# Optimization experiments

Measured on AMD Instinct MI355X. Metric: run time of the kernel, lower is better.

The kernel has to match this reference:

```python
import jax, jax.numpy as jnp
import numpy as np
import math

B, T, D, N = 4, 1024, 768, 7  # batch, seq, d_model, n_chambers
STEP, WARMUP = 4000, 2000      # curriculum: step past warmup -> all masks ~1
INIT_SCALE = 0.01


def _curriculum_masks():
    # NautilusScheduler.get_masks: smooth sigmoid activation per chamber (static floats)
    slope = 8.0 * N / WARMUP
    return [1.0 / (1.0 + math.exp(-slope * (STEP - WARMUP * (i + 0.5) / N))) for i in range(N)]


def _layernorm(x, g, b, eps=1e-5):
    m = jnp.mean(x, axis=-1, keepdims=True)
    v = jnp.mean((x - m) ** 2, axis=-1, keepdims=True)
    return (x - m) * jax.lax.rsqrt(v + eps) * g + b


def _chamber(h, Wq, Wk, gw, gb, sp, mask_val, causal):
    # get_bias stand-in: bilinear content bias (B,T,T)
    q = h @ Wq                                   # (B,T,D)
    k = h @ Wk                                   # (B,T,D)
    bias = jnp.einsum('btd,bsd->bts', q, k) / jnp.sqrt(jnp.asarray(D, h.dtype))
    bias = jnp.where(causal[None], bias, -jnp.inf)   # causal masked_fill
    w = jnp.nan_to_num(jax.nn.softmax(bias, axis=-1))
    enrichment = jnp.einsum('bts,bsd->btd', w, h) - h
    gate = jax.nn.sigmoid(h @ gw[:, None] + gb)      # (B,T,1)
    scale = jax.nn.softplus(sp)                      # learnable positive scale
    return scale * gate * mask_val * enrichment


def setup_inputs() -> dict:
    key = jax.random.key(0)
    ks = jax.random.split(key, 8)
    x = jax.random.normal(ks[0], (B, T, D), jnp.float32)
    s = 1.0 / np.sqrt(D)
    Wq = jax.random.normal(ks[1], (N, D, D), jnp.float32) * s
    Wk = jax.random.normal(ks[2], (N, D, D), jnp.float32) * s
    gate_w = jax.random.normal(ks[3], (N, D), jnp.float32) * 0.02
    gate_b = jnp.zeros((N,), jnp.float32)
    # per-chamber softplus-inverse init: log(exp(init*(1+3*prog))-1+1e-6)
    sp = np.array([math.log(math.exp(INIT_SCALE * (1.0 + 3.0 * i / (N - 1))) - 1.0 + 1e-6)
                   for i in range(N)], dtype=np.float32)
    scale_p = jnp.asarray(sp)
    merge_W = jax.random.normal(ks[4], (D, N * D), jnp.float32) * (1.0 / np.sqrt(N * D))
    return {
        'x': x, 'Wq': Wq, 'Wk': Wk, 'gate_w': gate_w, 'gate_b': gate_b,
        'scale_p': scale_p, 'merge_W': merge_W,
        'mode_logit': jnp.float32(0.0), 'residual_gate': jnp.float32(0.1),
        'ln_pre_g': jnp.ones((D,), jnp.float32), 'ln_pre_b': jnp.zeros((D,), jnp.float32),
        'ln_post_g': jnp.ones((D,), jnp.float32), 'ln_post_b': jnp.zeros((D,), jnp.float32),
    }


def reference(x, Wq, Wk, gate_w, gate_b, scale_p, merge_W, mode_logit,
              residual_gate, ln_pre_g, ln_pre_b, ln_post_g, ln_post_b):
    masks = _curriculum_masks()
    causal = jnp.tril(jnp.ones((T, T), bool))
    h = _layernorm(x, ln_pre_g, ln_pre_b)
    mode_gate = jax.nn.sigmoid(mode_logit)
    seq = jnp.zeros_like(h)
    deltas = []
    for i in range(N):  # fixed small structural loop over chambers
        seq = seq + _chamber(h + seq, Wq[i], Wk[i], gate_w[i], gate_b[i],
                             scale_p[i], masks[i], causal)
        deltas.append(_chamber(h, Wq[i], Wk[i], gate_w[i], gate_b[i],
                               scale_p[i], masks[i], causal))
    par = jnp.concatenate(deltas, axis=-1) @ merge_W.T  # (B,T,D)
    enrichment = (1.0 - mode_gate) * seq + mode_gate * par
    enrichment = _layernorm(enrichment, ln_post_g, ln_post_b)
    return x + residual_gate * enrichment
```

## Files before the change

### kernel.cpp

```cpp
#include <hip/hip_runtime.h>
#include <hip/hip_bf16.h>
#include <math.h>

#define D_MODEL 768
#define T_SEQ   1024
#define BATCH   4
#define NCH     7
#define ROWS    4096
#define KM      (NCH * D_MODEL)

typedef unsigned short u16;
typedef __attribute__((ext_vector_type(8))) short bh8;
typedef __attribute__((ext_vector_type(4))) float f32x4;

__device__ __forceinline__ u16 f2bf(float f) {
    union { float f; unsigned u; } v; v.f = f;
    return (u16)((v.u + 0x7fffu + ((v.u >> 16) & 1u)) >> 16);
}
__device__ __forceinline__ float bf2f(u16 b) {
    union { unsigned u; float f; } v; v.u = ((unsigned)b) << 16;
    return v.f;
}
__device__ __forceinline__ float wred_sum(float v) {
    #pragma unroll
    for (int o = 32; o; o >>= 1) v += __shfl_down(v, o, 64);
    return v;
}
__device__ __forceinline__ float wred_max(float v) {
    #pragma unroll
    for (int o = 32; o; o >>= 1) v = fmaxf(v, __shfl_down(v, o, 64));
    return v;
}
__device__ __forceinline__ float chamber_mask(int i) {
    float slope = 8.0f * 7.0f / 2000.0f;
    return 1.0f / (1.0f + __expf(-slope * (4000.0f - 2000.0f * (i + 0.5f) / 7.0f)));
}

#define GLD16(g, l) __builtin_amdgcn_global_load_lds( \
    (const __attribute__((address_space(1))) void*)(g), \
    (__attribute__((address_space(3))) void*)(l), 16, 0, 0)

__device__ __forceinline__ int xcd_swizzle(int gflat, int Ntot) {
    if ((Ntot & 7) == 0) {
        int chunk = Ntot >> 3;
        gflat = (gflat & 7) * chunk + (gflat >> 3);
    }
    return gflat;
}

__global__ __launch_bounds__(256)
void gemm_nt_kernel(const u16* __restrict__ A, const u16* __restrict__ B,
                    void* __restrict__ Cv,
                    int K, int lda, int ldb, int ldc,
                    long long sA1, long long sA2, long long sB1, long long sB2,
                    long long sC1, long long sC2, int zm,
                    float alpha, int mode, int causal_skip, int causal_k,
                    int kss, int klen)
{
    int gx = gridDim.x, gy = gridDim.y;
    int Ntot = gx * gy * gridDim.z;
    int gflat = xcd_swizzle(blockIdx.x + gx * (blockIdx.y + gy * blockIdx.z), Ntot);
    int bn = gflat % gx;
    int rest = gflat / gx;
    int bm = rest % gy;
    int bz = rest / gy;
    if (causal_skip && bn > bm) return;
    int bz1 = bz % zm, bz2 = bz / zm;

    const u16* Ab = A + bz1 * sA1 + bz2 * sA2 + (long long)(bm * 128) * lda;
    const u16* Bb = B + bz1 * sB1 + bz2 * sB2 + (long long)(bn * 128) * ldb;

    __shared__ u16 sm[4 * 128 * 32];
    u16* Al0 = sm;
    u16* Bl0 = sm + 128 * 32;
    u16* Al1 = sm + 2 * 128 * 32;
    u16* Bl1 = sm + 3 * 128 * 32;

    int tid  = threadIdx.x;
    int lane = tid & 63;
    int wave = tid >> 6;
    int wm = wave >> 1, wn = wave & 1;

    int k_begin = kss ? bz1 * kss : 0;
    int k_end   = klen ? (k_begin + klen) : K;
    if (causal_k) k_end = min(k_end, (bm + 1) * 128);

    f32x4 acc[4][4];
    #pragma unroll
    for (int i = 0; i < 4; i++)
        #pragma unroll
        for (int j = 0; j < 4; j++)
            acc[i][j] = (f32x4){0.f, 0.f, 0.f, 0.f};

    int srow = lane >> 2;
    int skq  = (lane & 3) * 8;
    int fm   = lane & 15;
    int fk   = (lane >> 4) * 8;

    for (int k0 = k_begin; k0 < k_end; k0 += 64) {
        __syncthreads();
        #pragma unroll
        for (int r = 0; r < 2; r++) {
            int row = r * 64 + wave * 16 + srow;
            long long ra = (long long)row * lda + k0 + skq;
            long long rb2 = (long long)row * ldb + k0 + skq;
            GLD16(Ab + ra,       Al0 + row * 32 + skq);
            GLD16(Bb + rb2,      Bl0 + row * 32 + skq);
            GLD16(Ab + ra + 32,  Al1 + row * 32 + skq);
            GLD16(Bb + rb2 + 32, Bl1 + row * 32 + skq);
        }
        __syncthreads();

        #pragma unroll
        for (int p = 0; p < 2; p++) {
            const u16* Al = p ? Al1 : Al0;
            const u16* Bl = p ? Bl1 : Bl0;
            bh8 af[4], bf[4];
            #pragma unroll
            for (int i = 0; i < 4; i++)
                af[i] = *(const bh8*)(Al + (wm * 64 + i * 16 + fm) * 32 + fk);
            #pragma unroll
            for (int j = 0; j < 4; j++)
                bf[j] = *(const bh8*)(Bl + (wn * 64 + j * 16 + fm) * 32 + fk);
            #pragma unroll
            for (int i = 0; i < 4; i++)
                #pragma unroll
                for (int j = 0; j < 4; j++)
                    acc[i][j] = __builtin_amdgcn_mfma_f32_16x16x32_bf16(af[i], bf[j], acc[i][j], 0, 0, 0);
        }
    }

    int rbase = bm * 128 + wm * 64 + (lane >> 4) * 4;
    int cbase = bn * 128 + wn * 64 + (lane & 15);
    long long zoff = bz1 * sC1 + bz2 * sC2;
    if (mode == 1) {
        u16* C = (u16*)Cv + zoff;
        #pragma unroll
        for (int i = 0; i < 4; i++)
            #pragma unroll
            for (int j = 0; j < 4; j++)
                #pragma unroll
                for (int r = 0; r < 4; r++)
                    C[(long long)(rbase + i * 16 + r) * ldc + cbase + j * 16] = f2bf(acc[i][j][r] * alpha);
    } else if (mode == 3) {
        u16* C = (u16*)Cv + zoff;
        #pragma unroll
        for (int i = 0; i < 4; i++)
            #pragma unroll
            for (int j = 0; j < 4; j++)
                #pragma unroll
                for (int r = 0; r < 4; r++) {
                    union { _Float16 h; u16 u; } cv;
                    cv.h = (_Float16)(acc[i][j][r] * alpha);
                    C[(long long)(rbase + i * 16 + r) * ldc + cbase + j * 16] = cv.u;
                }
    } else {
        float* C = (float*)Cv + zoff;
        #pragma unroll
        for (int i = 0; i < 4; i++)
            #pragma unroll
            for (int j = 0; j < 4; j++)
                #pragma unroll
                for (int r = 0; r < 4; r++)
                    C[(long long)(rbase + i * 16 + r) * ldc + cbase + j * 16] = acc[i][j][r] * alpha;
    }
}

__global__ __launch_bounds__(256)
void gemm64_nt_kernel(const u16* __restrict__ A, const u16* __restrict__ B,
                      void* __restrict__ Cv,
                      int K, int lda, int ldb, int ldc,
                      long long sA1, long long sA2, long long sB1, long long sB2,
                      long long sC1, long long sC2, int zm,
                      float alpha, int mode, int causal_skip, int causal_k,
                      float* __restrict__ hhfp, const float* __restrict__ coefp,
                      u16* __restrict__ hbsp, u16* __restrict__ htsp,
                      const float* __restrict__ hp, u16* __restrict__ dbp)
{
    int gx = gridDim.x, gy = gridDim.y;
    int Ntot = gx * gy * gridDim.z;
    int gflat = xcd_swizzle(blockIdx.x + gx * (blockIdx.y + gy * blockIdx.z), Ntot);
    int bn = gflat % gx;
    int rest = gflat / gx;
    int bm = rest % gy;
    int bz = rest / gy;
    if (causal_skip && bn > bm) return;
    int bz1 = bz % zm, bz2 = bz / zm;

    const u16* Ab = A + bz1 * sA1 + bz2 * sA2 + (long long)(bm * 64) * lda;
    const u16* Bb = B + bz1 * sB1 + bz2 * sB2 + (long long)(bn * 64) * ldb;

    __shared__ u16 sm[8 * 64 * 32];
    const int PS = 64 * 32;

    int tid  = threadIdx.x;
    int lane = tid & 63;
    int wave = tid >> 6;

    int k_end = causal_k ? min(K, (bm + 1) * 64) : K;

    f32x4 acc[4];
    #pragma unroll
    for (int j = 0; j < 4; j++) acc[j] = (f32x4){0.f, 0.f, 0.f, 0.f};

    int srow   = tid >> 2;
    int schunk = (tid & 3) * 8;
    int fm     = lane & 15;
    int fk     = (lane >> 4) * 8;

    int k0 = 0;
    while (k0 < k_end) {
        __syncthreads();
        if (k_end - k0 >= 128) {
            #pragma unroll
            for (int p = 0; p < 4; p++) {
                long long ra  = (long long)srow * lda + k0 + p * 32 + schunk;
                long long rb2 = (long long)srow * ldb + k0 + p * 32 + schunk;
                GLD16(Ab + ra,  sm + (2 * p) * PS + srow * 32 + schunk);
                GLD16(Bb + rb2, sm + (2 * p + 1) * PS + srow * 32 + schunk);
            }
            __syncthreads();
            #pragma unroll
            for (int p = 0; p < 4; p++) {
                const u16* Al = sm + (2 * p) * PS;
                const u16* Bl = sm + (2 * p + 1) * PS;
                bh8 af = *(const bh8*)(Al + (wave * 16 + fm) * 32 + fk);
                bh8 bf[4];
                #pragma unroll
                for (int j = 0; j < 4; j++)
                    bf[j] = *(const bh8*)(Bl + (j * 16 + fm) * 32 + fk);
                #pragma unroll
                for (int j = 0; j < 4; j++)
                    acc[j] = __builtin_amdgcn_mfma_f32_16x16x32_bf16(af, bf[j], acc[j], 0, 0, 0);
            }
            k0 += 128;
        } else {
            #pragma unroll
            for (int p = 0; p < 2; p++) {
                long long ra  = (long long)srow * lda + k0 + p * 32 + schunk;
                long long rb2 = (long long)srow * ldb + k0 + p * 32 + schunk;
                GLD16(Ab + ra,  sm + (2 * p) * PS + srow * 32 + schunk);
                GLD16(Bb + rb2, sm + (2 * p + 1) * PS + srow * 32 + schunk);
            }
            __syncthreads();
            #pragma unroll
            for (int p = 0; p < 2; p++) {
                const u16* Al = sm + (2 * p) * PS;
                const u16* Bl = sm + (2 * p + 1) * PS;
                bh8 af = *(const bh8*)(Al + (wave * 16 + fm) * 32 + fk);
                bh8 bf[4];
                #pragma unroll
                for (int j = 0; j < 4; j++)
                    bf[j] = *(const bh8*)(Bl + (j * 16 + fm) * 32 + fk);
                #pragma unroll
                for (int j = 0; j < 4; j++)
                    acc[j] = __builtin_amdgcn_mfma_f32_16x16x32_bf16(af, bf[j], acc[j], 0, 0, 0);
            }
            k0 += 64;
        }
    }

    int rbase = bm * 64 + wave * 16 + (lane >> 4) * 4;
    int cbase = bn * 64 + (lane & 15);
    long long zoff = bz1 * sC1 + bz2 * sC2;
    if (mode == 1) {
        u16* C = (u16*)Cv + zoff;
        #pragma unroll
        for (int j = 0; j < 4; j++)
            #pragma unroll
            for (int r = 0; r < 4; r++)
                C[(long long)(rbase + r) * ldc + cbase + j * 16] = f2bf(acc[j][r] * alpha);
    } else if (mode == 3) {
        u16* C = (u16*)Cv + zoff;
        #pragma unroll
        for (int j = 0; j < 4; j++)
            #pragma unroll
            for (int r = 0; r < 4; r++) {
                union { _Float16 h; u16 u; } cv;
                cv.h = (_Float16)(acc[j][r] * alpha);
                C[(long long)(rbase + r) * ldc + cbase + j * 16] = cv.u;
            }
    } else if (mode == 5) {
        int b = bz1, ch = bz2;
        #pragma unroll
        for (int r = 0; r < 4; r++) {
            int t = rbase + r;
            long long rowg = (long long)b * T_SEQ + t;
            float cf = coefp[(long long)ch * ROWS + rowg];
            #pragma unroll
            for (int j = 0; j < 4; j++) {
                int d = cbase + j * 16;
                float hv = hp[rowg * D_MODEL + d];
                dbp[rowg * KM + ch * D_MODEL + d] = f2bf(cf * (acc[j][r] - hv));
            }
        }
    } else if (mode == 6) {
        __syncthreads();
        u16* tile = sm;
        #pragma unroll
        for (int r = 0; r < 4; r++) {
            int t = rbase + r;
            long long rowg = (long long)bz1 * T_SEQ + t;
            float cf = coefp[rowg];
            int tl = t - bm * 64;
            #pragma unroll
            for (int j = 0; j < 4; j++) {
                int d = cbase + j * 16;
                long long idx = rowg * D_MODEL + d;
                float v = hhfp[idx];
                float nh = v + cf * (acc[j][r] - v);
                hhfp[idx] = nh;
                u16 w = f2bf(nh);
                hbsp[idx] = w;
                tile[((lane & 15) + j * 16) * 66 + tl] = w;
            }
        }
        __syncthreads();
        int dl = tid >> 2, tch = (tid & 3) * 16;
        long long ob = (long long)bz1 * T_SEQ * D_MODEL +
                       (long long)(bn * 64 + dl) * T_SEQ + bm * 64 + tch;
        #pragma unroll
        for (int kk = 0; kk < 16; kk++)
            htsp[ob + kk] = tile[dl * 66 + tch + kk];
    } else {
        float* C = (float*)Cv + zoff;
        #pragma unroll
        for (int j = 0; j < 4; j++)
            #pragma unroll
            for (int r = 0; r < 4; r++)
                C[(long long)(rbase + r) * ldc + cbase + j * 16] = acc[j][r] * alpha;
    }
}

__global__ __launch_bounds__(256)
void ln_pre_kernel(const float* __restrict__ x, const float* __restrict__ g,
                   const float* __restrict__ b, float* __restrict__ h,
                   float* __restrict__ hhf, u16* __restrict__ hbp,
                   u16* __restrict__ hbs)
{
    int row = blockIdx.x;
    long long base = (long long)row * D_MODEL;
    int tid = threadIdx.x, lane = tid & 63, wave = tid >> 6;
    __shared__ float red[4];
    float v[3]; float s = 0.f;
    #pragma unroll
    for (int k = 0; k < 3; k++) { v[k] = x[base + tid + k * 256]; s += v[k]; }
    s = wred_sum(s);
    if (lane == 0) red[wave] = s;
    __syncthreads();
    float mean = (red[0] + red[1] + red[2] + red[3]) * (1.f / D_MODEL);
    __syncthreads();
    float sq = 0.f;
    #pragma unroll
    for (int k = 0; k < 3; k++) { float dd = v[k] - mean; sq += dd * dd; }
    sq = wred_sum(sq);
    if (lane == 0) red[wave] = sq;
    __syncthreads();
    float var = (red[0] + red[1] + red[2] + red[3]) * (1.f / D_MODEL);
    float rstd = rsqrtf(var + 1e-5f);
    #pragma unroll
    for (int k = 0; k < 3; k++) {
        int c = tid + k * 256;
        float o = (v[k] - mean) * rstd * g[c] + b[c];
        h[base + c] = o; hhf[base + c] = o;
        u16 w = f2bf(o);
        hbp[base + c] = w; hbs[base + c] = w;
    }
}

__global__ __launch_bounds__(256)
void transpose2_kernel(const u16* __restrict__ hb, u16* __restrict__ htp,
                       u16* __restrict__ hts)
{
    __shared__ u16 tile[32][33];
    int b = blockIdx.z;
    int d0 = blockIdx.x * 32, t0 = blockIdx.y * 32;
    int tx = threadIdx.x & 31, ty = threadIdx.x >> 5;
    long long bb = (long long)b * T_SEQ * D_MODEL;
    #pragma unroll
    for (int i = 0; i < 32; i += 8)
        tile[ty + i][tx] = hb[bb + (long long)(t0 + ty + i) * D_MODEL + d0 + tx];
    __syncthreads();
    #pragma unroll
    for (int i = 0; i < 32; i += 8) {
        long long o = bb + (long long)(d0 + ty + i) * T_SEQ + t0 + tx;
        u16 w = tile[tx][ty + i];
        htp[o] = w; hts[o] = w;
    }
}

__device__ __forceinline__ void softmax_row(u16* row, int len, int tid, int lane, int wave,
                                            float* red)
{
    float ev[4];
    float m = -3.0e38f;
    #pragma unroll
    for (int k = 0; k < 4; k++) {
        int s = tid + k * 256;
        if (s < len) {
            union { u16 u; _Float16 h; } cv; cv.u = row[s];
            ev[k] = (float)cv.h;
        } else ev[k] = -3.0e38f;
        m = fmaxf(m, ev[k]);
    }
    m = wred_max(m);
    if (lane == 0) red[wave] = m;
    __syncthreads();
    m = fmaxf(fmaxf(red[0], red[1]), fmaxf(red[2], red[3]));
    __syncthreads();
    float sum = 0.f;
    #pragma unroll
    for (int k = 0; k < 4; k++) {
        int s = tid + k * 256;
        float e = (s < len) ? __expf(ev[k] - m) : 0.f;
        ev[k] = e; sum += e;
    }
    sum = wred_sum(sum);
    if (lane == 0) red[wave] = sum;
    __syncthreads();
    sum = red[0] + red[1] + red[2] + red[3];
    float inv = 1.f / sum;
    #pragma unroll
    for (int k = 0; k < 4; k++)
        row[tid + k * 256] = f2bf(ev[k] * inv);
}

__global__ __launch_bounds__(256)
void softmax_kernel(u16* __restrict__ SP)
{
    int t = blockIdx.x, z = blockIdx.y;
    __shared__ float red[4];
    int tid = threadIdx.x, lane = tid & 63, wave = tid >> 6;
    softmax_row(SP + (long long)z * T_SEQ * T_SEQ + (long long)t * T_SEQ,
                t + 1, tid, lane, wave, red);
}

__global__ __launch_bounds__(256)
void softmax_coef_kernel(u16* __restrict__ SP, const float* __restrict__ hhf,
                         const float* __restrict__ gw, const float* __restrict__ gb,
                         const float* __restrict__ sp, int ci,
                         float* __restrict__ coefS)
{
    int t = blockIdx.x, z = blockIdx.y;
    int tid = threadIdx.x, lane = tid & 63, wave = tid >> 6;
    if (z == BATCH) {
        int row = t * 4 + wave;
        long long base = (long long)row * D_MODEL;
        const float* g = gw + ci * D_MODEL;
        float dot = 0.f;
        #pragma unroll
        for (int k = 0; k < 12; k++) dot += hhf[base + lane + 64 * k] * g[lane + 64 * k];
        dot = wred_sum(dot);
        if (lane == 0) {
            float gate = 1.f / (1.f + __expf(-(dot + gb[ci])));
            coefS[row] = log1pf(expf(sp[ci])) * chamber_mask(ci) * gate;
        }
        return;
    }
    __shared__ float red[4];
    softmax_row(SP + (long long)z * T_SEQ * T_SEQ + (long long)t * T_SEQ,
                t + 1, tid, lane, wave, red);
}

__global__ __launch_bounds__(256)
void coef_par_kernel(const float* __restrict__ h, const float* __restrict__ gw,
                     const float* __restrict__ gb, const float* __restrict__ sp,
                     float* __restrict__ coefP)
{
    int row = blockIdx.x * 4 + (threadIdx.x >> 6);
    int lane = threadIdx.x & 63;
    long long base = (long long)row * D_MODEL;
    float hv[12];
    #pragma unroll
    for (int k = 0; k < 12; k++) hv[k] = h[base + lane + 64 * k];
    for (int ci = 0; ci < NCH; ci++) {
        const float* g = gw + ci * D_MODEL;
        float dot = 0.f;
        #pragma unroll
        for (int k = 0; k < 12; k++) dot += hv[k] * g[lane + 64 * k];
        dot = wred_sum(dot);
        if (lane == 0) {
            float gate = 1.f / (1.f + __expf(-(dot + gb[ci])));
            coefP[ci * ROWS + row] = log1pf(expf(sp[ci])) * chamber_mask(ci) * gate;
        }
    }
}

__global__ __launch_bounds__(256)
void cast4_kernel(const float4* __restrict__ in, ushort4* __restrict__ outp, int n4)
{
    int i = blockIdx.x * 256 + threadIdx.x;
    if (i < n4) {
        float4 v = in[i];
        ushort4 o;
        o.x = f2bf(v.x); o.y = f2bf(v.y); o.z = f2bf(v.z); o.w = f2bf(v.w);
        outp[i] = o;
    }
}

__global__ __launch_bounds__(256)
void final_kernel(const float* __restrict__ x, const float* __restrict__ h,
                  const float* __restrict__ hhf, const u16* __restrict__ Pp,
                  const float* __restrict__ mode_logit, const float* __restrict__ residual_gate,
                  const float* __restrict__ g, const float* __restrict__ b,
                  float* __restrict__ out)
{
    const long long RDe = (long long)ROWS * D_MODEL;
    int row = blockIdx.x;
    long long base = (long long)row * D_MODEL;
    int tid = threadIdx.x, lane = tid & 63, wave = tid >> 6;
    __shared__ float red[4];
    float mg = 1.f / (1.f + __expf(-mode_logit[0]));
    float rg = residual_gate[0];
    float e[3]; float s = 0.f;
    #pragma unroll
    for (int k = 0; k < 3; k++) {
        int c = tid + k * 256;
        float p = 0.f;
        #pragma unroll
        for (int z = 0; z < NCH; z++) p += bf2f(Pp[z * RDe + base + c]);
        float v = (1.f - mg) * (hhf[base + c] - h[base + c]) + mg * p;
        e[k] = v; s += v;
    }
    s = wred_sum(s);
    if (lane == 0) red[wave] = s;
    __syncthreads();
    float mean = (red[0] + red[1] + red[2] + red[3]) * (1.f / D_MODEL);
    __syncthreads();
    float sq = 0.f;
    #pragma unroll
    for (int k = 0; k < 3; k++) { float dd = e[k] - mean; sq += dd * dd; }
    sq = wred_sum(sq);
    if (lane == 0) red[wave] = sq;
    __syncthreads();
    float var = (red[0] + red[1] + red[2] + red[3]) * (1.f / D_MODEL);
    float rstd = rsqrtf(var + 1e-5f);
    #pragma unroll
    for (int k = 0; k < 3; k++) {
        int c = tid + k * 256;
        out[base + c] = x[base + c] + rg * ((e[k] - mean) * rstd * g[c] + b[c]);
    }
}

extern "C" void kernel_launch(void* const* d_in, const int* in_sizes, int n_in,
                              void* d_out, int out_size, void* d_ws, size_t ws_size,
                              hipStream_t stream)
{
    (void)in_sizes; (void)n_in; (void)out_size; (void)ws_size;
    const float* x             = (const float*)d_in[0];
    const float* Wq            = (const float*)d_in[1];
    const float* Wk            = (const float*)d_in[2];
    const float* gate_w        = (const float*)d_in[3];
    const float* gate_b        = (const float*)d_in[4];
    const float* scale_p       = (const float*)d_in[5];
    const float* merge_W       = (const float*)d_in[6];
    const float* mode_logit    = (const float*)d_in[7];
    const float* residual_gate = (const float*)d_in[8];
    const float* ln_pre_g      = (const float*)d_in[9];
    const float* ln_pre_b      = (const float*)d_in[10];
    const float* ln_post_g     = (const float*)d_in[11];
    const float* ln_post_b     = (const float*)d_in[12];
    float* out = (float*)d_out;

    const long long DD  = (long long)D_MODEL * D_MODEL;
    const long long TD  = (long long)T_SEQ * D_MODEL;
    const long long TTs = (long long)T_SEQ * T_SEQ;
    const long long RDe = (long long)ROWS * D_MODEL;

    size_t off = 0;
    char* wsb = (char*)d_ws;
    auto alloc = [&](size_t bytes) -> void* {
        void* p = wsb + off; off += (bytes + 255) & ~(size_t)255; return p;
    };
    u16*   Mtb  = (u16*)alloc((size_t)NCH * DD * 2);
    u16*   mgb  = (u16*)alloc((size_t)D_MODEL * KM * 2);
    float* h    = (float*)alloc(RDe * 4);
    float* hhf  = (float*)alloc(RDe * 4);
    u16*   hbp  = (u16*)alloc(RDe * 2);
    u16*   htp  = (u16*)alloc(RDe * 2);
    u16*   hbs  = (u16*)alloc(RDe * 2);
    u16*   hts0 = (u16*)alloc(RDe * 2);
    u16*   hts1 = (u16*)alloc(RDe * 2);
    u16*   Spar = (u16*)alloc((size_t)(NCH * BATCH) * TTs * 2);
    u16*   Sseq = (u16*)alloc((size_t)BATCH * TTs * 2);
    u16*   Upar = (u16*)alloc((size_t)NCH * RDe * 2);
    u16*   Useq = (u16*)alloc(RDe * 2);
    u16*   db   = (u16*)alloc((size_t)ROWS * KM * 2);
    float* coefP= (float*)alloc((size_t)NCH * ROWS * 4);
    float* coefS= (float*)alloc((size_t)ROWS * 4);
    u16*   Wqb  = Spar;
    u16*   Wkb  = Spar + (size_t)NCH * DD;
    u16*   Pp   = Upar;

    const float sc = 1.0f / sqrtf((float)D_MODEL);
    const int N4W = (int)((size_t)NCH * DD) / 4;
    const int N4M = (int)((size_t)D_MODEL * KM) / 4;

    ln_pre_kernel<<<ROWS, 256, 0, stream>>>(x, ln_pre_g, ln_pre_b, h, hhf, hbp, hbs);
    cast4_kernel<<<(N4W + 255) / 256, 256, 0, stream>>>((const float4*)Wq, (ushort4*)Wqb, N4W);
    cast4_kernel<<<(N4W + 255) / 256, 256, 0, stream>>>((const float4*)Wk, (ushort4*)Wkb, N4W);
    cast4_kernel<<<(N4M + 255) / 256, 256, 0, stream>>>((const float4*)merge_W, (ushort4*)mgb, N4M);
    transpose2_kernel<<<dim3(24, 32, BATCH), 256, 0, stream>>>(hbp, htp, hts0);
    coef_par_kernel<<<ROWS / 4, 256, 0, stream>>>(h, gate_w, gate_b, scale_p, coefP);

    gemm_nt_kernel<<<dim3(6, 6, NCH), 256, 0, stream>>>(
        Wkb, Wqb, Mtb, D_MODEL, D_MODEL, D_MODEL, D_MODEL,
        DD, 0, DD, 0, DD, 0, NCH, 1.f, 1, 0, 0, 0, 0);

    gemm_nt_kernel<<<dim3(6, 32, NCH), 256, 0, stream>>>(
        hbp, Mtb, Upar, D_MODEL, D_MODEL, D_MODEL, D_MODEL,
        0, 0, DD, 0, RDe, 0, NCH, 1.f, 1, 0, 0, 0, 0);
    gemm64_nt_kernel<<<dim3(16, 16, BATCH * NCH), 256, 0, stream>>>(
        Upar, hbp, Spar, D_MODEL, D_MODEL, D_MODEL, T_SEQ,
        TD, RDe, TD, 0, TTs, 4 * TTs, BATCH, sc, 3, 1, 0,
        nullptr, nullptr, nullptr, nullptr, nullptr, nullptr);
    softmax_kernel<<<dim3(T_SEQ, BATCH * NCH), 256, 0, stream>>>(Spar);
    gemm64_nt_kernel<<<dim3(12, 16, BATCH * NCH), 256, 0, stream>>>(
        Spar, htp, nullptr, T_SEQ, T_SEQ, T_SEQ, D_MODEL,
        TTs, 4 * TTs, TD, 0, 0, 0, BATCH, 1.f, 5, 0, 1,
        nullptr, coefP, nullptr, nullptr, h, db);
    gemm_nt_kernel<<<dim3(6, 32, NCH), 256, 0, stream>>>(
        db, mgb, Pp, KM, KM, KM, D_MODEL,
        0, 0, 0, 0, RDe, 0, NCH, 1.f, 1, 0, 0, D_MODEL, D_MODEL);

    u16* htsCur = hts0;
    u16* htsNxt = hts1;
    for (int i = 0; i < NCH; i++) {
        gemm64_nt_kernel<<<dim3(12, 64, 1), 256, 0, stream>>>(
            hbs, Mtb + (long long)i * DD, Useq,
            D_MODEL, D_MODEL, D_MODEL, D_MODEL, 0, 0, 0, 0, 0, 0, 1,
            1.f, 1, 0, 0, nullptr, nullptr, nullptr, nullptr, nullptr, nullptr);
        gemm64_nt_kernel<<<dim3(16, 16, BATCH), 256, 0, stream>>>(
            Useq, hbs, Sseq, D_MODEL, D_MODEL, D_MODEL, T_SEQ,
            TD, 0, TD, 0, TTs, 0, BATCH, sc, 3, 1, 0,
            nullptr, nullptr, nullptr, nullptr, nullptr, nullptr);
        softmax_coef_kernel<<<dim3(T_SEQ, BATCH + 1), 256, 0, stream>>>(
            Sseq, hhf, gate_w, gate_b, scale_p, i, coefS);
        gemm64_nt_kernel<<<dim3(12, 16, BATCH), 256, 0, stream>>>(
            Sseq, htsCur, nullptr, T_SEQ, T_SEQ, T_SEQ, D_MODEL,
            TTs, 0, TD, 0, 0, 0, BATCH, 1.f, 6, 0, 1,
            hhf, coefS, hbs, htsNxt, nullptr, nullptr);
        u16* tmp = htsCur; htsCur = htsNxt; htsNxt = tmp;
    }

    final_kernel<<<ROWS, 256, 0, stream>>>(x, h, hhf, Pp, mode_logit, residual_gate,
                                           ln_post_g, ln_post_b, out);
}
```

Baseline: 790.8 us.

## Interleave parallel-branch chamber GEMMs into sequential-loop launches via multi-descriptor kernels

Replaces the separate batched parallel-branch launches (U, scores, softmax, PV, merge) with per-chamber slices that are co-launched inside the sequential chamber loop. New gemm128_tri/gemm64_tri kernels take up to three GEMM descriptors and route block ids to each one, so the small, latency-bound sequential GEMMs share a grid with independent parallel work. The merge GEMM is split per chamber and lagged by one iteration. The goal is better GPU occupancy during the serial dependency chain and fewer launches. In exchange the merge GEMM runs as smaller pieces and the parallel work is spread across more launches.

```diff
diff --git a/kernel.cpp b/kernel.cpp
--- a/kernel.cpp
+++ b/kernel.cpp
@@ -1,5 +1,4 @@
 #include <hip/hip_runtime.h>
-#include <hip/hip_bf16.h>
 #include <math.h>
 
 #define D_MODEL 768
@@ -48,29 +47,44 @@
     return gflat;
 }
 
-__global__ __launch_bounds__(256)
-void gemm_nt_kernel(const u16* __restrict__ A, const u16* __restrict__ B,
-                    void* __restrict__ Cv,
-                    int K, int lda, int ldb, int ldc,
-                    long long sA1, long long sA2, long long sB1, long long sB2,
-                    long long sC1, long long sC2, int zm,
-                    float alpha, int mode, int causal_skip, int causal_k,
-                    int kss, int klen)
-{
-    int gx = gridDim.x, gy = gridDim.y;
-    int Ntot = gx * gy * gridDim.z;
-    int gflat = xcd_swizzle(blockIdx.x + gx * (blockIdx.y + gy * blockIdx.z), Ntot);
-    int bn = gflat % gx;
-    int rest = gflat / gx;
-    int bm = rest % gy;
-    int bz = rest / gy;
-    if (causal_skip && bn > bm) return;
-    int bz1 = bz % zm, bz2 = bz / zm;
-
-    const u16* Ab = A + bz1 * sA1 + bz2 * sA2 + (long long)(bm * 128) * lda;
-    const u16* Bb = B + bz1 * sB1 + bz2 * sB2 + (long long)(bn * 128) * ldb;
-
-    __shared__ u16 sm[4 * 128 * 32];
+struct GDesc {
+    const u16* A; const u16* B; void* C;
+    const float* coef;
+    const float* hfrz;
+    float* hhf;
+    u16* hbs;
+    u16* hts;
+    u16* db;
+    long long sA1, sB1, sC1;
+    int K, lda, ldb, ldc;
+    int gx, gy, gz;
+    int mode, cskip, ck;
+    float alpha;
+};
+
+__device__ __forceinline__ bool g_route(const GDesc& d, int& id,
+                                        int& bn, int& bm, int& bz)
+{
+    int n = d.gx * d.gy * d.gz;
+    if (id < n) {
+        int s = xcd_swizzle(id, n);
+        bn = s % d.gx;
+        int r = s / d.gx;
+        bm = r % d.gy;
+        bz = r / d.gy;
+        return true;
+    }
+    id -= n;
+    return false;
+}
+
+__device__ void g128_body(const GDesc& d, u16* sm, int bn, int bm, int bz)
+{
+    if (d.cskip && bn > bm) return;
+
+    const u16* Ab = d.A + bz * d.sA1 + (long long)(bm * 128) * d.lda;
+    const u16* Bb = d.B + bz * d.sB1 + (long long)(bn * 128) * d.ldb;
+
     u16* Al0 = sm;
     u16* Bl0 = sm + 128 * 32;
     u16* Al1 = sm + 2 * 128 * 32;
@@ -81,9 +95,7 @@
     int wave = tid >> 6;
     int wm = wave >> 1, wn = wave & 1;
 
-    int k_begin = kss ? bz1 * kss : 0;
-    int k_end   = klen ? (k_begin + klen) : K;
-    if (causal_k) k_end = min(k_end, (bm + 1) * 128);
+    int k_end = d.ck ? min(d.K, (bm + 1) * 128) : d.K;
 
     f32x4 acc[4][4];
     #pragma unroll
@@ -97,13 +109,13 @@
     int fm   = lane & 15;
     int fk   = (lane >> 4) * 8;
 
-    for (int k0 = k_begin; k0 < k_end; k0 += 64) {
+    for (int k0 = 0; k0 < k_end; k0 += 64) {
         __syncthreads();
         #pragma unroll
         for (int r = 0; r < 2; r++) {
             int row = r * 64 + wave * 16 + srow;
-            long long ra = (long long)row * lda + k0 + skq;
-            long long rb2 = (long long)row * ldb + k0 + skq;
+            long long ra  = (long long)row * d.lda + k0 + skq;
+            long long rb2 = (long long)row * d.ldb + k0 + skq;
             GLD16(Ab + ra,       Al0 + row * 32 + skq);
             GLD16(Bb + rb2,      Bl0 + row * 32 + skq);
             GLD16(Ab + ra + 32,  Al1 + row * 32 + skq);
@@ -132,72 +144,52 @@
 
     int rbase = bm * 128 + wm * 64 + (lane >> 4) * 4;
     int cbase = bn * 128 + wn * 64 + (lane & 15);
-    long long zoff = bz1 * sC1 + bz2 * sC2;
-    if (mode == 1) {
-        u16* C = (u16*)Cv + zoff;
+    long long zoff = (long long)bz * d.sC1;
+    if (d.mode == 1) {
+        u16* C = (u16*)d.C + zoff;
         #pragma unroll
         for (int i = 0; i < 4; i++)
             #pragma unroll
             for (int j = 0; j < 4; j++)
                 #pragma unroll
                 for (int r = 0; r < 4; r++)
-                    C[(long long)(rbase + i * 16 + r) * ldc + cbase + j * 16] = f2bf(acc[i][j][r] * alpha);
-    } else if (mode == 3) {
-        u16* C = (u16*)Cv + zoff;
-        #pragma unroll
-        for (int i = 0; i < 4; i++)
-            #pragma unroll
-            for (int j = 0; j < 4; j++)
-                #pragma unroll
-                for (int r = 0; r < 4; r++) {
-                    union { _Float16 h; u16 u; } cv;
-                    cv.h = (_Float16)(acc[i][j][r] * alpha);
-                    C[(long long)(rbase + i * 16 + r) * ldc + cbase + j * 16] = cv.u;
-                }
+                    C[(long long)(rbase + i * 16 + r) * d.ldc + cbase + j * 16] = f2bf(acc[i][j][r] * d.alpha);
     } else {
-        float* C = (float*)Cv + zoff;
+        float* C = (float*)d.C + zoff;
         #pragma unroll
         for (int i = 0; i < 4; i++)
             #pragma unroll
             for (int j = 0; j < 4; j++)
                 #pragma unroll
                 for (int r = 0; r < 4; r++)
-                    C[(long long)(rbase + i * 16 + r) * ldc + cbase + j * 16] = acc[i][j][r] * alpha;
-    }
-}
-
-__global__ __launch_bounds__(256)
-void gemm64_nt_kernel(const u16* __restrict__ A, const u16* __restrict__ B,
-                      void* __restrict__ Cv,
-                      int K, int lda, int ldb, int ldc,
-                      long long sA1, long long sA2, long long sB1, long long sB2,
-                      long long sC1, long long sC2, int zm,
-                      float alpha, int mode, int causal_skip, int causal_k,
-                      float* __restrict__ hhfp, const float* __restrict__ coefp,
-                      u16* __restrict__ hbsp, u16* __restrict__ htsp,
-                      const float* __restrict__ hp, u16* __restrict__ dbp)
-{
-    int gx = gridDim.x, gy = gridDim.y;
-    int Ntot = gx * gy * gridDim.z;
-    int gflat = xcd_swizzle(blockIdx.x + gx * (blockIdx.y + gy * blockIdx.z), Ntot);
-    int bn = gflat % gx;
-    int rest = gflat / gx;
-    int bm = rest % gy;
-    int bz = rest / gy;
-    if (causal_skip && bn > bm) return;
-    int bz1 = bz % zm, bz2 = bz / zm;
-
-    const u16* Ab = A + bz1 * sA1 + bz2 * sA2 + (long long)(bm * 64) * lda;
-    const u16* Bb = B + bz1 * sB1 + bz2 * sB2 + (long long)(bn * 64) * ldb;
-
-    __shared__ u16 sm[8 * 64 * 32];
+                    C[(long long)(rbase + i * 16 + r) * d.ldc + cbase + j * 16] = acc[i][j][r] * d.alpha;
+    }
+}
+
+__global__ __launch_bounds__(256)
+void gemm128_tri(GDesc d0, GDesc d1, GDesc d2)
+{
+    __shared__ u16 sm[4 * 128 * 32];
+    int id = blockIdx.x, bn, bm, bz;
+    if (g_route(d0, id, bn, bm, bz)) { g128_body(d0, sm, bn, bm, bz); return; }
+    if (g_route(d1, id, bn, bm, bz)) { g128_body(d1, sm, bn, bm, bz); return; }
+    if (g_route(d2, id, bn, bm, bz)) { g128_body(d2, sm, bn, bm, bz); return; }
+}
+
+__device__ void g64_body(const GDesc& d, u16* sm, int bn, int bm, int bz)
+{
+    if (d.cskip && bn > bm) return;
+
+    const u16* Ab = d.A + bz * d.sA1 + (long long)(bm * 64) * d.lda;
+    const u16* Bb = d.B + bz * d.sB1 + (long long)(bn * 64) * d.ldb;
+
     const int PS = 64 * 32;
 
     int tid  = threadIdx.x;
     int lane = tid & 63;
     int wave = tid >> 6;
 
-    int k_end = causal_k ? min(K, (bm + 1) * 64) : K;
+    int k_end = d.ck ? min(d.K, (bm + 1) * 64) : d.K;
 
     f32x4 acc[4];
     #pragma unroll
@@ -214,8 +206,8 @@
         if (k_end - k0 >= 128) {
             #pragma unroll
             for (int p = 0; p < 4; p++) {
-                long long ra  = (long long)srow * lda + k0 + p * 32 + schunk;
-                long long rb2 = (long long)srow * ldb + k0 + p * 32 + schunk;
+                long long ra  = (long long)srow * d.lda + k0 + p * 32 + schunk;
+                long long rb2 = (long long)srow * d.ldb + k0 + p * 32 + schunk;
                 GLD16(Ab + ra,  sm + (2 * p) * PS + srow * 32 + schunk);
                 GLD16(Bb + rb2, sm + (2 * p + 1) * PS + srow * 32 + schunk);
             }
@@ -237,8 +229,8 @@
         } else {
             #pragma unroll
             for (int p = 0; p < 2; p++) {
-                long long ra  = (long long)srow * lda + k0 + p * 32 + schunk;
-                long long rb2 = (long long)srow * ldb + k0 + p * 32 + schunk;
+                long long ra  = (long long)srow * d.lda + k0 + p * 32 + schunk;
+                long long rb2 = (long long)srow * d.ldb + k0 + p * 32 + schunk;
                 GLD16(Ab + ra,  sm + (2 * p) * PS + srow * 32 + schunk);
                 GLD16(Bb + rb2, sm + (2 * p + 1) * PS + srow * 32 + schunk);
             }
@@ -262,74 +254,83 @@
 
     int rbase = bm * 64 + wave * 16 + (lane >> 4) * 4;
     int cbase = bn * 64 + (lane & 15);
-    long long zoff = bz1 * sC1 + bz2 * sC2;
-    if (mode == 1) {
-        u16* C = (u16*)Cv + zoff;
+    long long zoff = (long long)bz * d.sC1;
+    if (d.mode == 1) {
+        u16* C = (u16*)d.C + zoff;
         #pragma unroll
         for (int j = 0; j < 4; j++)
             #pragma unroll
             for (int r = 0; r < 4; r++)
-                C[(long long)(rbase + r) * ldc + cbase + j * 16] = f2bf(acc[j][r] * alpha);
-    } else if (mode == 3) {
-        u16* C = (u16*)Cv + zoff;
+                C[(long long)(rbase + r) * d.ldc + cbase + j * 16] = f2bf(acc[j][r] * d.alpha);
+    } else if (d.mode == 3) {
+        u16* C = (u16*)d.C + zoff;
         #pragma unroll
         for (int j = 0; j < 4; j++)
             #pragma unroll
             for (int r = 0; r < 4; r++) {
                 union { _Float16 h; u16 u; } cv;
-                cv.h = (_Float16)(acc[j][r] * alpha);
-                C[(long long)(rbase + r) * ldc + cbase + j * 16] = cv.u;
+                cv.h = (_Float16)(acc[j][r] * d.alpha);
+                C[(long long)(rbase + r) * d.ldc + cbase + j * 16] = cv.u;
             }
-    } else if (mode == 5) {
-        int b = bz1, ch = bz2;
+    } else if (d.mode == 5) {
         #pragma unroll
         for (int r = 0; r < 4; r++) {
             int t = rbase + r;
-            long long rowg = (long long)b * T_SEQ + t;
-            float cf = coefp[(long long)ch * ROWS + rowg];
+            long long rowg = (long long)bz * T_SEQ + t;
+            float cf = d.coef[rowg];
             #pragma unroll
             for (int j = 0; j < 4; j++) {
-                int d = cbase + j * 16;
-                float hv = hp[rowg * D_MODEL + d];
-                dbp[rowg * KM + ch * D_MODEL + d] = f2bf(cf * (acc[j][r] - hv));
+                int dc = cbase + j * 16;
+                float hv = d.hfrz[rowg * D_MODEL + dc];
+                d.db[rowg * KM + dc] = f2bf(cf * (acc[j][r] - hv));
             }
         }
-    } else if (mode == 6) {
+    } else if (d.mode == 6) {
         __syncthreads();
         u16* tile = sm;
         #pragma unroll
         for (int r = 0; r < 4; r++) {
             int t = rbase + r;
-            long long rowg = (long long)bz1 * T_SEQ + t;
-            float cf = coefp[rowg];
+            long long rowg = (long long)bz * T_SEQ + t;
+            float cf = d.coef[rowg];
             int tl = t - bm * 64;
             #pragma unroll
             for (int j = 0; j < 4; j++) {
-                int d = cbase + j * 16;
-                long long idx = rowg * D_MODEL + d;
-                float v = hhfp[idx];
+                int dc = cbase + j * 16;
+                long long idx = rowg * D_MODEL + dc;
+                float v = d.hhf[idx];
                 float nh = v + cf * (acc[j][r] - v);
-                hhfp[idx] = nh;
+                d.hhf[idx] = nh;
                 u16 w = f2bf(nh);
-                hbsp[idx] = w;
+                d.hbs[idx] = w;
                 tile[((lane & 15) + j * 16) * 66 + tl] = w;
             }
         }
         __syncthreads();
         int dl = tid >> 2, tch = (tid & 3) * 16;
-        long long ob = (long long)bz1 * T_SEQ * D_MODEL +
+        long long ob = (long long)bz * T_SEQ * D_MODEL +
                        (long long)(bn * 64 + dl) * T_SEQ + bm * 64 + tch;
         #pragma unroll
         for (int kk = 0; kk < 16; kk++)
-            htsp[ob + kk] = tile[dl * 66 + tch + kk];
+            d.hts[ob + kk] = tile[dl * 66 + tch + kk];
     } else {
-        float* C = (float*)Cv + zoff;
+        float* C = (float*)d.C + zoff;
         #pragma unroll
         for (int j = 0; j < 4; j++)
             #pragma unroll
             for (int r = 0; r < 4; r++)
-                C[(long long)(rbase + r) * ldc + cbase + j * 16] = acc[j][r] * alpha;
-    }
+                C[(long long)(rbase + r) * d.ldc + cbase + j * 16] = acc[j][r] * d.alpha;
+    }
+}
+
+__global__ __launch_bounds__(256)
+void gemm64_tri(GDesc d0, GDesc d1, GDesc d2)
+{
+    __shared__ u16 sm[8 * 64 * 32];
+    int id = blockIdx.x, bn, bm, bz;
+    if (g_route(d0, id, bn, bm, bz)) { g64_body(d0, sm, bn, bm, bz); return; }
+    if (g_route(d1, id, bn, bm, bz)) { g64_body(d1, sm, bn, bm, bz); return; }
+    if (g_route(d2, id, bn, bm, bz)) { g64_body(d2, sm, bn, bm, bz); return; }
 }
 
 __global__ __launch_bounds__(256)
@@ -426,24 +427,16 @@
 }
 
 __global__ __launch_bounds__(256)
-void softmax_kernel(u16* __restrict__ SP)
-{
-    int t = blockIdx.x, z = blockIdx.y;
-    __shared__ float red[4];
-    int tid = threadIdx.x, lane = tid & 63, wave = tid >> 6;
-    softmax_row(SP + (long long)z * T_SEQ * T_SEQ + (long long)t * T_SEQ,
-                t + 1, tid, lane, wave, red);
-}
-
-__global__ __launch_bounds__(256)
-void softmax_coef_kernel(u16* __restrict__ SP, const float* __restrict__ hhf,
-                         const float* __restrict__ gw, const float* __restrict__ gb,
-                         const float* __restrict__ sp, int ci,
-                         float* __restrict__ coefS)
-{
+void softmax9_kernel(u16* __restrict__ Sseq, u16* __restrict__ SparI,
+                     const float* __restrict__ hhf, const float* __restrict__ gw,
+                     const float* __restrict__ gb, const float* __restrict__ sp,
+                     int ci, float* __restrict__ coefS)
+{
+    const long long TTs = (long long)T_SEQ * T_SEQ;
     int t = blockIdx.x, z = blockIdx.y;
     int tid = threadIdx.x, lane = tid & 63, wave = tid >> 6;
-    if (z == BATCH) {
+    __shared__ float red[4];
+    if (z == 4) {
         int row = t * 4 + wave;
         long long base = (long long)row * D_MODEL;
         const float* g = gw + ci * D_MODEL;
@@ -457,9 +450,9 @@
         }
         return;
     }
-    __shared__ float red[4];
-    softmax_row(SP + (long long)z * T_SEQ * T_SEQ + (long long)t * T_SEQ,
-                t + 1, tid, lane, wave, red);
+    u16* base = (z < 4) ? (Sseq + (long long)z * TTs)
+                        : (SparI + (long long)(z - 5) * TTs);
+    softmax_row(base + (long long)t * T_SEQ, t + 1, tid, lane, wave, red);
 }
 
 __global__ __launch_bounds__(256)
@@ -596,6 +589,20 @@
     const int N4W = (int)((size_t)NCH * DD) / 4;
     const int N4M = (int)((size_t)D_MODEL * KM) / 4;
 
+    auto mkg = [](const u16* A, const u16* B, void* C,
+                  long long sA1, long long sB1, long long sC1,
+                  int K, int lda, int ldb, int ldc,
+                  int gx, int gy, int gz, int mode, int cskip, int ck, float alpha) {
+        GDesc d{};
+        d.A = A; d.B = B; d.C = C;
+        d.sA1 = sA1; d.sB1 = sB1; d.sC1 = sC1;
+        d.K = K; d.lda = lda; d.ldb = ldb; d.ldc = ldc;
+        d.gx = gx; d.gy = gy; d.gz = gz;
+        d.mode = mode; d.cskip = cskip; d.ck = ck; d.alpha = alpha;
+        return d;
+    };
+    GDesc ez{};
+
     ln_pre_kernel<<<ROWS, 256, 0, stream>>>(x, ln_pre_g, ln_pre_b, h, hhf, hbp, hbs);
     cast4_kernel<<<(N4W + 255) / 256, 256, 0, stream>>>((const float4*)Wq, (ushort4*)Wqb, N4W);
     cast4_kernel<<<(N4W + 255) / 256, 256, 0, stream>>>((const float4*)Wk, (ushort4*)Wkb, N4W);
@@ -603,44 +610,53 @@
     transpose2_kernel<<<dim3(24, 32, BATCH), 256, 0, stream>>>(hbp, htp, hts0);
     coef_par_kernel<<<ROWS / 4, 256, 0, stream>>>(h, gate_w, gate_b, scale_p, coefP);
 
-    gemm_nt_kernel<<<dim3(6, 6, NCH), 256, 0, stream>>>(
-        Wkb, Wqb, Mtb, D_MODEL, D_MODEL, D_MODEL, D_MODEL,
-        DD, 0, DD, 0, DD, 0, NCH, 1.f, 1, 0, 0, 0, 0);
-
-    gemm_nt_kernel<<<dim3(6, 32, NCH), 256, 0, stream>>>(
-        hbp, Mtb, Upar, D_MODEL, D_MODEL, D_MODEL, D_MODEL,
-        0, 0, DD, 0, RDe, 0, NCH, 1.f, 1, 0, 0, 0, 0);
-    gemm64_nt_kernel<<<dim3(16, 16, BATCH * NCH), 256, 0, stream>>>(
-        Upar, hbp, Spar, D_MODEL, D_MODEL, D_MODEL, T_SEQ,
-        TD, RDe, TD, 0, TTs, 4 * TTs, BATCH, sc, 3, 1, 0,
-        nullptr, nullptr, nullptr, nullptr, nullptr, nullptr);
-    softmax_kernel<<<dim3(T_SEQ, BATCH * NCH), 256, 0, stream>>>(Spar);
-    gemm64_nt_kernel<<<dim3(12, 16, BATCH * NCH), 256, 0, stream>>>(
-        Spar, htp, nullptr, T_SEQ, T_SEQ, T_SEQ, D_MODEL,
-        TTs, 4 * TTs, TD, 0, 0, 0, BATCH, 1.f, 5, 0, 1,
-        nullptr, coefP, nullptr, nullptr, h, db);
-    gemm_nt_kernel<<<dim3(6, 32, NCH), 256, 0, stream>>>(
-        db, mgb, Pp, KM, KM, KM, D_MODEL,
-        0, 0, 0, 0, RDe, 0, NCH, 1.f, 1, 0, 0, D_MODEL, D_MODEL);
+    {
+        GDesc dmt = mkg(Wkb, Wqb, Mtb, DD, DD, DD,
+                        D_MODEL, D_MODEL, D_MODEL, D_MODEL, 6, 6, NCH, 1, 0, 0, 1.f);
+        gemm128_tri<<<dim3(6 * 6 * NCH), 256, 0, stream>>>(dmt, ez, ez);
+    }
 
     u16* htsCur = hts0;
     u16* htsNxt = hts1;
     for (int i = 0; i < NCH; i++) {
-        gemm64_nt_kernel<<<dim3(12, 64, 1), 256, 0, stream>>>(
-            hbs, Mtb + (long long)i * DD, Useq,
-            D_MODEL, D_MODEL, D_MODEL, D_MODEL, 0, 0, 0, 0, 0, 0, 1,
-            1.f, 1, 0, 0, nullptr, nullptr, nullptr, nullptr, nullptr, nullptr);
-        gemm64_nt_kernel<<<dim3(16, 16, BATCH), 256, 0, stream>>>(
-            Useq, hbs, Sseq, D_MODEL, D_MODEL, D_MODEL, T_SEQ,
-            TD, 0, TD, 0, TTs, 0, BATCH, sc, 3, 1, 0,
-            nullptr, nullptr, nullptr, nullptr, nullptr, nullptr);
-        softmax_coef_kernel<<<dim3(T_SEQ, BATCH + 1), 256, 0, stream>>>(
-            Sseq, hhf, gate_w, gate_b, scale_p, i, coefS);
-        gemm64_nt_kernel<<<dim3(12, 16, BATCH), 256, 0, stream>>>(
-            Sseq, htsCur, nullptr, T_SEQ, T_SEQ, T_SEQ, D_MODEL,
-            TTs, 0, TD, 0, 0, 0, BATCH, 1.f, 6, 0, 1,
-            hhf, coefS, hbs, htsNxt, nullptr, nullptr);
+        GDesc dU  = mkg(hbs, Mtb + (long long)i * DD, Useq, 0, 0, 0,
+                        D_MODEL, D_MODEL, D_MODEL, D_MODEL, 6, 32, 1, 1, 0, 0, 1.f);
+        GDesc dPU = mkg(hbp, Mtb + (long long)i * DD, Upar + (long long)i * RDe, 0, 0, 0,
+                        D_MODEL, D_MODEL, D_MODEL, D_MODEL, 6, 32, 1, 1, 0, 0, 1.f);
+        GDesc dMg = ez;
+        if (i >= 1)
+            dMg = mkg(db + (long long)(i - 1) * D_MODEL, mgb + (long long)(i - 1) * D_MODEL,
+                      Pp + (long long)(i - 1) * RDe, 0, 0, 0,
+                      D_MODEL, KM, KM, D_MODEL, 6, 32, 1, 1, 0, 0, 1.f);
+        int nU = 192 * (i >= 1 ? 3 : 2);
+        gemm128_tri<<<dim3(nU), 256, 0, stream>>>(dU, dPU, dMg);
+
+        GDesc dS  = mkg(Useq, hbs, Sseq, TD, TD, TTs,
+                        D_MODEL, D_MODEL, D_MODEL, T_SEQ, 16, 16, BATCH, 3, 1, 0, sc);
+        GDesc dPS = mkg(Upar + (long long)i * RDe, hbp, Spar + (long long)i * BATCH * TTs,
+                        TD, TD, TTs,
+                        D_MODEL, D_MODEL, D_MODEL, T_SEQ, 16, 16, BATCH, 3, 1, 0, sc);
+        gemm64_tri<<<dim3(2048), 256, 0, stream>>>(dS, dPS, ez);
+
+        softmax9_kernel<<<dim3(T_SEQ, 9), 256, 0, stream>>>(
+            Sseq, Spar + (long long)i * BATCH * TTs, hhf, gate_w, gate_b, scale_p, i, coefS);
+
+        GDesc dPV = mkg(Sseq, htsCur, nullptr, TTs, TD, 0,
+                        T_SEQ, T_SEQ, T_SEQ, 0, 12, 16, BATCH, 6, 0, 1, 1.f);
+        dPV.hhf = hhf; dPV.coef = coefS; dPV.hbs = hbs; dPV.hts = htsNxt;
+        GDesc dPPV = mkg(Spar + (long long)i * BATCH * TTs, htp, nullptr, TTs, TD, 0,
+                         T_SEQ, T_SEQ, T_SEQ, 0, 12, 16, BATCH, 5, 0, 1, 1.f);
+        dPPV.coef = coefP + (long long)i * ROWS; dPPV.hfrz = h;
+        dPPV.db = db + (long long)i * D_MODEL;
+        gemm64_tri<<<dim3(1536), 256, 0, stream>>>(dPV, dPPV, ez);
+
         u16* tmp = htsCur; htsCur = htsNxt; htsNxt = tmp;
+    }
+
+    {
+        GDesc dM6 = mkg(db + 6LL * D_MODEL, mgb + 6LL * D_MODEL, Pp + 6LL * RDe, 0, 0, 0,
+                        D_MODEL, KM, KM, D_MODEL, 12, 64, 1, 1, 0, 0, 1.f);
+        gemm64_tri<<<dim3(768), 256, 0, stream>>>(dM6, ez, ez);
     }
 
     final_kernel<<<ROWS, 256, 0, stream>>>(x, h, hhf, Pp, mode_logit, residual_gate,
```

New measurement: 879.0 us. +11.2%, slower.
